# Performance work log

Measured on AMD Instinct MI355X. Metric: run time of the kernel, lower is better.

Reference implementation:

```python
import jax, jax.numpy as jnp
import numpy as np
from jax import lax

N, K, T_OBS, PRED = 64, 48, 30, 15
EMB, NODE, EDGE, ATT, CNN = 64, 128, 256, 64, 512


def setup_inputs():
    key = jax.random.key(0)
    ks = jax.random.split(key, 18)
    rn = lambda k, s, sc=1.0: jax.random.normal(k, s, jnp.float32) * sc
    return {
        "img_embedding": rn(ks[0], (N, CNN)),
        "target_obs_pos_abs": rn(ks[1], (N, T_OBS, 2)),
        "target_obs_pos_rel": rn(ks[2], (N, T_OBS, 2)),
        "target_obs_pos_step": rn(ks[3], (N, T_OBS, 2), 0.1),
        "nearby_obs_pos_abs": rn(ks[4], (N, K, T_OBS, 2)),
        "nearby_obs_pos_rel": rn(ks[5], (N, K, T_OBS, 2)),
        "nearby_obs_pos_step": rn(ks[6], (N, K, T_OBS, 2), 0.1),
        "target_obs_hist_size": jax.random.randint(ks[7], (N, 1), 0, T_OBS),
        "nearby_obs_hist_sizes": jax.random.randint(ks[8], (N, K, 1), 0, T_OBS),
        "W_disp": rn(ks[9], (EMB, 2), 0.1), "b_disp": jnp.zeros((EMB,), jnp.float32),
        "Wih_t": rn(ks[10], (4 * NODE, EMB), 0.05), "Whh_t": rn(ks[11], (4 * NODE, NODE), 0.05),
        "bih_t": jnp.zeros((4 * NODE,), jnp.float32), "bhh_t": jnp.zeros((4 * NODE,), jnp.float32),
        "Wih_n": rn(ks[12], (4 * EDGE, EMB), 0.05), "Whh_n": rn(ks[13], (4 * EDGE, EDGE), 0.05),
        "bih_n": jnp.zeros((4 * EDGE,), jnp.float32), "bhh_n": jnp.zeros((4 * EDGE,), jnp.float32),
        "W_att_t": rn(ks[14], (ATT, 2), 0.1), "b_att_t": jnp.zeros((ATT,), jnp.float32),
        "W_att_n": rn(ks[15], (ATT, 2), 0.1), "b_att_n": jnp.zeros((ATT,), jnp.float32),
        "W_pred": rn(ks[16], (2, NODE + CNN + EDGE), 0.02), "b_pred": jnp.zeros((2,), jnp.float32),
    }


def _lstm_cell(x, h, c, Wih, Whh, bih, bhh):
    # PyTorch LSTM gate order: i, f, g, o
    g = x @ Wih.T + h @ Whh.T + bih + bhh
    i, f, gg, o = jnp.split(g, 4, axis=-1)
    c2 = jax.nn.sigmoid(f) * c + jax.nn.sigmoid(i) * jnp.tanh(gg)
    return jax.nn.sigmoid(o) * jnp.tanh(c2), c2


def _forward(img_embedding, target_obs_pos_abs, target_obs_pos_rel, target_obs_pos_step,
             nearby_obs_pos_abs, nearby_obs_pos_rel, nearby_obs_pos_step,
             W_disp, b_disp, Wih_t, Whh_t, bih_t, bhh_t, Wih_n, Whh_n, bih_n, bhh_n,
             W_att_t, b_att_t, W_att_n, b_att_n, W_pred, b_pred,
             target_obs_hist_size, nearby_obs_hist_sizes):
    t_hist = target_obs_hist_size[:, 0]          # [N]
    n_hist = nearby_obs_hist_sizes[:, :, 0]      # [N, K]
    M = N * K

    def step(carry, t):
        tht, tct, nht, nct, Ht, cabs, crel, cstep, nabs, nstep = carry
        is_obs = t < T_OBS
        tc = jnp.minimum(t, T_OBS - 1)
        # prediction branch (only takes effect when t >= T_OBS)
        pred_out = jnp.concatenate([tht, img_embedding, Ht], 1) @ W_pred.T + b_pred  # [N,2]
        cabs = jnp.where(is_obs, target_obs_pos_abs[:, tc], cabs + pred_out)
        crel = jnp.where(is_obs, target_obs_pos_rel[:, tc], crel + pred_out)
        cstep = jnp.where(is_obs, target_obs_pos_step[:, tc], pred_out)
        nabs = jnp.where(is_obs, nearby_obs_pos_abs[:, :, tc], nabs)
        nstep = jnp.where(is_obs, nearby_obs_pos_step[:, :, tc], nstep)
        tmask = jnp.where(is_obs, t_hist > T_OBS - t, True)   # [N] bool
        nmask = jnp.where(is_obs, n_hist > T_OBS - t, True)   # [N,K] bool
        gate_t = jnp.sum(tmask) > 0  # emulates 'continue' when no target observed
        # target LSTM step, masked scatter-back
        th2, tc2 = _lstm_cell(cstep @ W_disp.T + b_disp, tht, tct, Wih_t, Whh_t, bih_t, bhh_t)
        u = (tmask & gate_t)[:, None]
        tht = jnp.where(u, th2, tht)
        tct = jnp.where(u, tc2, tct)
        # nearby LSTM step, masked scatter-back
        currN = jnp.sum(nmask)
        gate_n = gate_t & (currN > 0)
        nh2, nc2 = _lstm_cell(nstep.reshape(M, 2) @ W_disp.T + b_disp, nht, nct, Wih_n, Whh_n, bih_n, bhh_n)
        un = (nmask.reshape(M) & gate_n)[:, None]
        nht = jnp.where(un, nh2, nht)
        nct = jnp.where(un, nc2, nct)
        # social attention over padded nearby dim
        an = (nabs - cabs[:, None, :]) @ W_att_n.T + b_att_n   # [N,K,ATT]
        at = crel @ W_att_t.T + b_att_t                        # [N,ATT]
        mf = nmask.astype(jnp.float32)
        sc = jnp.einsum('nka,na->nk', an, at) * currN.astype(jnp.float32) / jnp.sqrt(jnp.float32(ATT))
        sc = sc * mf
        num = jnp.exp(sc - jnp.max(sc, 1, keepdims=True)) * mf
        w = num / (jnp.sum(num, 1, keepdims=True) + 1e-6)
        Ht = jnp.where(gate_n, jnp.einsum('nke,nk->ne', nht.reshape(N, K, EDGE), w), Ht)
        return (tht, tct, nht, nct, Ht, cabs, crel, cstep, nabs, nstep), crel

    z = lambda s: jnp.zeros(s, jnp.float32)
    init = (z((N, NODE)), z((N, NODE)), z((M, EDGE)), z((M, EDGE)), z((N, EDGE)),
            z((N, 2)), z((N, 2)), z((N, 2)), z((N, K, 2)), z((N, K, 2)))
    _, rels = lax.scan(step, init, jnp.arange(1, T_OBS + PRED))
    # last PRED emitted crel values are pred_traj[:, 0:PRED]
    return jnp.transpose(rels[-PRED:], (1, 0, 2))


def reference(img_embedding, target_obs_pos_abs, target_obs_pos_rel, target_obs_pos_step,
              nearby_obs_pos_abs, nearby_obs_pos_rel, nearby_obs_pos_step,
              target_obs_hist_size, nearby_obs_hist_sizes,
              W_disp, b_disp, Wih_t, Whh_t, bih_t, bhh_t, Wih_n, Whh_n, bih_n, bhh_n,
              W_att_t, b_att_t, W_att_n, b_att_n, W_pred, b_pred):
    return _forward(img_embedding, target_obs_pos_abs, target_obs_pos_rel, target_obs_pos_step,
                    nearby_obs_pos_abs, nearby_obs_pos_rel, nearby_obs_pos_step,
                    W_disp, b_disp, Wih_t, Whh_t, bih_t, bhh_t, Wih_n, Whh_n, bih_n, bhh_n,
                    W_att_t, b_att_t, W_att_n, b_att_n, W_pred, b_pred,
                    target_obs_hist_size, nearby_obs_hist_sizes)
```

## Files before the change

### kernel.cpp

```cpp
#include <hip/hip_runtime.h>
#include <math.h>

#define NT 64
#define KN 48
#define TOBS 30
#define NPRED 15
#define EMB 64
#define NODE 128
#define EDGE 256
#define ATTD 64
#define CNN 512
#define GNN 1024
#define GTT 512
#define KKA 320
#define TMAX 44

typedef _Float16 f16;
typedef f16 f16x8 __attribute__((ext_vector_type(8)));
typedef f16 f16x2 __attribute__((ext_vector_type(2)));
typedef float f32x4 __attribute__((ext_vector_type(4)));

__device__ __forceinline__ float rcp_f(float x) { return __builtin_amdgcn_rcpf(x); }
__device__ __forceinline__ float sigm(float x) { return rcp_f(1.f + __expf(-x)); }
__device__ __forceinline__ float tanh_f(float x) {
  float xx = fminf(fmaxf(x, -20.f), 20.f);
  float e = __expf(-2.f * xx);
  return (1.f - e) * rcp_f(1.f + e);
}
__device__ __forceinline__ unsigned ldcoh(const unsigned* p) {
  return __hip_atomic_load(p, __ATOMIC_RELAXED, __HIP_MEMORY_SCOPE_AGENT);
}
__device__ __forceinline__ float ldcohf(const float* p) {
  unsigned u = __hip_atomic_load((const unsigned*)p, __ATOMIC_RELAXED, __HIP_MEMORY_SCOPE_AGENT);
  return __builtin_bit_cast(float, u);
}
__device__ __forceinline__ void stcoh(unsigned* p, unsigned v) {
  __hip_atomic_store(p, v, __ATOMIC_RELAXED, __HIP_MEMORY_SCOPE_AGENT);
}
__device__ __forceinline__ void stcohf(float* p, float v) {
  __hip_atomic_store((unsigned*)p, __builtin_bit_cast(unsigned, v),
                     __ATOMIC_RELAXED, __HIP_MEMORY_SCOPE_AGENT);
}

__global__ __launch_bounds__(512) void prep_kernel(
    const float* __restrict__ Wih_n, const float* __restrict__ Whh_n,
    const float* __restrict__ bih_n, const float* __restrict__ bhh_n,
    const float* __restrict__ Wih_t, const float* __restrict__ Whh_t,
    const float* __restrict__ bih_t, const float* __restrict__ bhh_t,
    const int* __restrict__ t_hist, const int* __restrict__ n_hist,
    f16* __restrict__ Wn, f16* __restrict__ Wt,
    float* __restrict__ bias_n, float* __restrict__ bias_t,
    int* __restrict__ gt_arr, int* __restrict__ gn_arr, float* __restrict__ cn_arr,
    int* __restrict__ last29p, unsigned* __restrict__ flags)
{
  const int gid = blockIdx.x * 512 + threadIdx.x;
  const int nthr = gridDim.x * 512;
  __shared__ int sgn[TMAX + 1];

  if (gid < 2 * NT) flags[gid] = 0u;

  for (int idx = gid; idx < GNN * KKA; idx += nthr) {
    const int j    = idx & 7;
    const int lane = (idx >> 3) & 63;
    const int g    = (idx >> 9) & 3;
    const int r    = idx >> 11;
    const int kk   = r % 10;
    const int s    = r / 10;
    const int w    = s & 7;
    const int h    = s >> 3;
    const int col = g * 256 + h * 128 + w * 16 + (lane & 15);
    const int k   = kk * 32 + (lane >> 4) * 8 + j;
    const float v = (k < EMB) ? Wih_n[col * EMB + k] : Whh_n[col * EDGE + (k - EMB)];
    Wn[idx] = (f16)v;
  }
  for (int idx = gid; idx < GTT * 192; idx += nthr) {
    const int j = idx & 7;
    const int col = (idx >> 3) & 511;
    const int c8 = idx >> 12;
    const int k = c8 * 8 + j;
    const float v = (k < EMB) ? Wih_t[col * EMB + k] : Whh_t[col * NODE + (k - EMB)];
    Wt[idx] = (f16)v;
  }
  for (int idx = gid; idx < GNN; idx += nthr) bias_n[idx] = bih_n[idx] + bhh_n[idx];
  for (int idx = gid; idx < GTT; idx += nthr) bias_t[idx] = bih_t[idx] + bhh_t[idx];

  if (blockIdx.x == 0 && threadIdx.x < 352) {
    const int t = (threadIdx.x >> 3) + 1;
    const int part = threadIdx.x & 7;
    int any_t = 0, cnt = 0;
    if (t < TOBS) {
      const int thr = TOBS - t;
      for (int nn = part; nn < NT; nn += 8) any_t |= (t_hist[nn] > thr) ? 1 : 0;
      for (int m = part; m < NT * KN; m += 8) cnt += (n_hist[m] > thr) ? 1 : 0;
    } else { any_t = (part == 0); cnt = (part == 0) ? NT * KN : 0; }
    #pragma unroll
    for (int off = 1; off < 8; off <<= 1) {
      any_t |= __shfl_xor(any_t, off);
      cnt   += __shfl_xor(cnt, off);
    }
    if (part == 0) {
      const int gn = (any_t && cnt > 0) ? 1 : 0;
      gt_arr[t] = any_t;
      gn_arr[t] = gn;
      cn_arr[t] = (float)cnt;
      sgn[t] = gn;
    }
  }
  __syncthreads();
  if (blockIdx.x == 0 && threadIdx.x == 0) {
    int l = 30;
    for (int t = 29; t >= 1; --t) if (sgn[t]) { l = t; break; }
    last29p[0] = l;
  }
}

__global__ __launch_bounds__(512, 2) void model_kernel(
    const float* __restrict__ img, const float* __restrict__ tabs,
    const float* __restrict__ trel, const float* __restrict__ tstep,
    const float* __restrict__ nabs_g, const float* __restrict__ nstep_g,
    const int* __restrict__ thist_g, const int* __restrict__ nhist_g,
    const float* __restrict__ W_disp, const float* __restrict__ b_disp,
    const float* __restrict__ W_att_t, const float* __restrict__ b_att_t,
    const float* __restrict__ W_att_n, const float* __restrict__ b_att_n,
    const float* __restrict__ W_pred, const float* __restrict__ b_pred,
    const f16* __restrict__ Wn, const f16* __restrict__ Wt,
    const float* __restrict__ bias_n, const float* __restrict__ bias_t,
    const int* __restrict__ gt_arr, const int* __restrict__ gn_arr,
    const float* __restrict__ cn_arr, const int* __restrict__ last29p,
    unsigned* __restrict__ flags, unsigned* __restrict__ Hglob,
    float* __restrict__ Tglob,
    float* __restrict__ out)
{
  __shared__ f16 s_wlds[3 * 16384];
  __shared__ f16 Ax[KN][72];
  __shared__ f16 Ah[KN][264];
  __shared__ float s_tht[NODE];
  __shared__ float s_tct[64];
  __shared__ f16  s_th16[NODE];
  __shared__ float s_Ht[EDGE];
  __shared__ f16  s_x16[EMB];
  __shared__ float s_g[256];
  __shared__ float s_bt[256];
  __shared__ float s_at[ATTD];
  __shared__ float s_sc[KN], s_w[KN];
  __shared__ float s_scal[8];
  __shared__ float s_pimg[2];
  __shared__ int   s_nh[KN];
  __shared__ float s_wp[2][384];
  __shared__ float s_wan0[ATTD], s_wan1[ATTD], s_ban[ATTD];
  __shared__ float s_wat0[ATTD], s_wat1[ATTD], s_bat[ATTD];
  __shared__ float s_wd0[EMB], s_wd1[EMB], s_bd[EMB];

  const int tid  = threadIdx.x;
  const int n    = blockIdx.x & 63;
  const int hb   = blockIdx.x >> 6;
  const int w    = tid >> 6;
  const int lane = tid & 63;
  const int cl   = lane & 15;
  const int kq   = lane >> 4;
  const int koff = kq * 8;

  for (int i = tid; i < KN * 264; i += 512) ((f16*)Ah)[i] = (f16)0.f;
  for (int i = tid; i < NODE; i += 512) { s_tht[i] = 0.f; s_th16[i] = (f16)0.f; }
  if (tid < 64) s_tct[tid] = 0.f;
  for (int i = tid; i < EDGE; i += 512) s_Ht[i] = 0.f;
  if (tid < 256) {
    const int g = tid >> 6, dl = tid & 63;
    s_bt[tid] = bias_t[g * 128 + hb * 64 + dl];
  }
  for (int i = tid; i < 768; i += 512) {
    const int ww = i / 384, j = i - ww * 384;
    s_wp[ww][j] = (j < 128) ? W_pred[ww * 896 + j] : W_pred[ww * 896 + 640 + (j - 128)];
  }
  if (tid < KN) s_nh[tid] = nhist_g[n * KN + tid];
  if (tid < 8) s_scal[tid] = 0.f;
  if (tid >= 64 && tid < 128) {
    const int a = tid - 64;
    s_wan0[a] = W_att_n[a * 2]; s_wan1[a] = W_att_n[a * 2 + 1]; s_ban[a] = b_att_n[a];
  }
  if (tid >= 128 && tid < 192) {
    const int a = tid - 128;
    s_wat0[a] = W_att_t[a * 2]; s_wat1[a] = W_att_t[a * 2 + 1]; s_bat[a] = b_att_t[a];
  }
  if (tid >= 192 && tid < 256) {
    const int e = tid - 192;
    s_wd0[e] = W_disp[e * 2]; s_wd1[e] = W_disp[e * 2 + 1]; s_bd[e] = b_disp[e];
  }
  const int thist = thist_g[n];
  const int last29 = last29p[0];

  for (int i = tid; i < 3 * 8 * 256; i += 512) {
    const int c  = i & 255;
    const int wv = (i >> 8) & 7;
    const int kk = i >> 11;
    const size_t gbase = ((size_t)((hb * 8 + wv) * 10 + kk)) * 2048;
    *(f16x8*)(s_wlds + (size_t)(kk * 8 + wv) * 2048 + c * 8) =
        *(const f16x8*)(Wn + gbase + c * 8);
  }

  if (w < 2) {
    float s = 0.f;
    for (int j = lane; j < CNN; j += 64) s += img[n * CNN + j] * W_pred[w * 896 + 128 + j];
    for (int off = 32; off; off >>= 1) s += __shfl_down(s, off);
    if (lane == 0) s_pimg[w] = s + b_pred[w];
  }

  float creg[3][4];
  #pragma unroll
  for (int b = 0; b < 3; ++b)
    #pragma unroll
    for (int c = 0; c < 4; ++c) creg[b][c] = 0.f;

  float bias_q[4];
  #pragma unroll
  for (int g = 0; g < 4; ++g) bias_q[g] = bias_n[g * 256 + hb * 128 + w * 16 + cl];

  const f16* gW = Wn + ((size_t)(hb * 8 + w) * 10) * 2048 + (size_t)lane * 8;
  const f16* lW = s_wlds + (size_t)w * 2048 + (size_t)lane * 8;
  const int e_g = hb * 128 + w * 16 + cl;
  unsigned* myflag = flags + n * 2 + hb;
  unsigned* otflag = flags + n * 2 + (1 - hb);
  int bn = 0;

  __syncthreads();

  {
    for (int i = tid; i < KN * EMB; i += 512) {
      const int k = i >> 6, e = i & 63;
      const float s0 = nstep_g[((n * KN + k) * TOBS + 1) * 2 + 0];
      const float s1 = nstep_g[((n * KN + k) * TOBS + 1) * 2 + 1];
      Ax[k][e] = (f16)(s0 * s_wd0[e] + s1 * s_wd1[e] + s_bd[e]);
    }
    if (tid < 2) {
      s_scal[tid]     = tabs[(n * TOBS + 1) * 2 + tid];
      s_scal[2 + tid] = trel[(n * TOBS + 1) * 2 + tid];
      s_scal[4 + tid] = tstep[(n * TOBS + 1) * 2 + tid];
    }
    if (tid >= 448) {
      const int e = tid - 448;
      const float a0 = tstep[(n * TOBS + 1) * 2 + 0], a1 = tstep[(n * TOBS + 1) * 2 + 1];
      s_x16[e] = (f16)(a0 * s_wd0[e] + a1 * s_wd1[e] + s_bd[e]);
    }
    if (tid >= 384 && tid < 448) {
      const int a = tid - 384;
      const float r0 = trel[(n * TOBS + 1) * 2 + 0], r1 = trel[(n * TOBS + 1) * 2 + 1];
      s_at[a] = r0 * s_wat0[a] + r1 * s_wat1[a] + s_bat[a];
    }
  }
  __syncthreads();

  for (int t = 1; t <= TMAX; ++t) {
    const bool is_obs = (t < TOBS);
    const int tc = is_obs ? t : (TOBS - 1);
    const int gate_t = gt_arr[t];
    const int gate_n = gn_arr[t];
    const float currN = cn_arr[t];
    const bool tmask = is_obs ? (thist > (TOBS - t)) : true;
    const bool do_t = gate_t && tmask;
    const bool need_x = (gate_n || do_t);
    const bool do_att = gate_n && (t >= last29);
    const int par = bn & 1;

    if (!is_obs) {
      if (w < 2) {
        float s = 0.f;
        for (int j = lane; j < NODE; j += 64) s += s_tht[j] * s_wp[w][j];
        for (int j = lane; j < EDGE; j += 64) s += s_Ht[j] * s_wp[w][128 + j];
        for (int off = 32; off; off >>= 1) s += __shfl_down(s, off);
        if (lane == 0) {
          const float p = s + s_pimg[w];
          const float cabs = s_scal[w] + p;
          const float crel = s_scal[2 + w] + p;
          s_scal[w] = cabs; s_scal[2 + w] = crel; s_scal[4 + w] = p;
          if (hb == 0) out[(n * NPRED + (t - TOBS)) * 2 + w] = crel;
        }
      }
      __syncthreads();
      if (tid >= 448) {
        const int e = tid - 448;
        s_x16[e] = (f16)(s_scal[4] * s_wd0[e] + s_scal[5] * s_wd1[e] + s_bd[e]);
      }
      if (tid >= 384 && tid < 448) {
        const int a = tid - 384;
        s_at[a] = s_scal[2] * s_wat0[a] + s_scal[3] * s_wat1[a] + s_bat[a];
      }
      __syncthreads();
    }

    f16 hreg[3][4];
    if (gate_n) {
      f32x4 acc[3][4];
      #pragma unroll
      for (int rt = 0; rt < 3; ++rt)
        #pragma unroll
        for (int g = 0; g < 4; ++g) acc[rt][g] = (f32x4){0.f, 0.f, 0.f, 0.f};

      #pragma unroll
      for (int kk = 0; kk < 10; ++kk) {
        f16x8 bf[4];
        if (kk < 3) {
          #pragma unroll
          for (int g = 0; g < 4; ++g)
            bf[g] = *(const f16x8*)(lW + kk * 16384 + g * 512);
        } else {
          #pragma unroll
          for (int g = 0; g < 4; ++g)
            bf[g] = *(const f16x8*)(gW + kk * 2048 + g * 512);
        }
        f16x8 af[3];
        #pragma unroll
        for (int rt = 0; rt < 3; ++rt) {
          const int row = rt * 16 + cl;
          const f16* ap = (kk < 2) ? &Ax[row][kk * 32 + koff]
                                   : &Ah[row][(kk - 2) * 32 + koff];
          af[rt] = *(const f16x8*)ap;
        }
        #pragma unroll
        for (int g = 0; g < 4; ++g)
          #pragma unroll
          for (int rt = 0; rt < 3; ++rt)
            acc[rt][g] = __builtin_amdgcn_mfma_f32_16x16x32_f16(af[rt], bf[g], acc[rt][g], 0, 0, 0);
      }

      unsigned* Hg = Hglob + (size_t)(par * NT + n) * (KN * 128);
      #pragma unroll
      for (int rt = 0; rt < 3; ++rt) {
        #pragma unroll
        for (int jj = 0; jj < 4; ++jj) {
          const int row = rt * 16 + kq * 4 + jj;
          const bool nm = is_obs ? (s_nh[row] > (TOBS - t)) : true;
          f16 hv;
          if (nm) {
            const float iv = acc[rt][0][jj] + bias_q[0];
            const float fv = acc[rt][1][jj] + bias_q[1];
            const float gv = acc[rt][2][jj] + bias_q[2];
            const float ov = acc[rt][3][jj] + bias_q[3];
            const float c2 = sigm(fv) * creg[rt][jj] + sigm(iv) * tanh_f(gv);
            creg[rt][jj] = c2;
            hv = (f16)(sigm(ov) * tanh_f(c2));
          } else {
            hv = Ah[row][e_g];
          }
          hreg[rt][jj] = hv;
          const unsigned lo = (unsigned)__builtin_bit_cast(unsigned short, hv);
          const unsigned hi = (unsigned)__shfl_down((int)lo, 1);
          if (!(cl & 1))
            stcoh(Hg + row * 128 + (e_g >> 1), lo | (hi << 16));
        }
      }
    }

    if (do_t && tid < 256) {
      const int g = tid >> 6, dl = tid & 63;
      const int col = g * 128 + hb * 64 + dl;
      float g0 = s_bt[tid], g1 = 0.f, g2 = 0.f, g3 = 0.f;
      const f16x2* xt2 = (const f16x2*)s_x16;
      const f16x2* th2 = (const f16x2*)s_th16;
      const f16x8* wp = (const f16x8*)(Wt + col * 8);
      #pragma unroll
      for (int c8 = 0; c8 < 8; ++c8) {
        const f16x8 wv = wp[c8 * 512];
        f16x2 w0 = {wv[0], wv[1]}, w1 = {wv[2], wv[3]};
        f16x2 w2 = {wv[4], wv[5]}, w3 = {wv[6], wv[7]};
        g0 = __builtin_amdgcn_fdot2(w0, xt2[c8 * 4 + 0], g0, false);
        g1 = __builtin_amdgcn_fdot2(w1, xt2[c8 * 4 + 1], g1, false);
        g2 = __builtin_amdgcn_fdot2(w2, xt2[c8 * 4 + 2], g2, false);
        g3 = __builtin_amdgcn_fdot2(w3, xt2[c8 * 4 + 3], g3, false);
      }
      #pragma unroll
      for (int c8 = 8; c8 < 24; ++c8) {
        const f16x8 wv = wp[c8 * 512];
        f16x2 w0 = {wv[0], wv[1]}, w1 = {wv[2], wv[3]};
        f16x2 w2 = {wv[4], wv[5]}, w3 = {wv[6], wv[7]};
        g0 = __builtin_amdgcn_fdot2(w0, th2[(c8 - 8) * 4 + 0], g0, false);
        g1 = __builtin_amdgcn_fdot2(w1, th2[(c8 - 8) * 4 + 1], g1, false);
        g2 = __builtin_amdgcn_fdot2(w2, th2[(c8 - 8) * 4 + 2], g2, false);
        g3 = __builtin_amdgcn_fdot2(w3, th2[(c8 - 8) * 4 + 3], g3, false);
      }
      s_g[tid] = (g0 + g1) + (g2 + g3);
    }
    if (do_att && tid >= 256 && tid < 256 + KN) {
      const int k = tid - 256;
      const float a0 = nabs_g[((n * KN + k) * TOBS + tc) * 2 + 0] - s_scal[0];
      const float a1 = nabs_g[((n * KN + k) * TOBS + tc) * 2 + 1] - s_scal[1];
      const bool nm = is_obs ? (s_nh[k] > (TOBS - t)) : true;
      float c0 = 0.f, c1 = 0.f, c2 = 0.f, c3 = 0.f;
      #pragma unroll 4
      for (int a = 0; a < ATTD; a += 4) {
        c0 += (a0 * s_wan0[a]     + a1 * s_wan1[a]     + s_ban[a])     * s_at[a];
        c1 += (a0 * s_wan0[a + 1] + a1 * s_wan1[a + 1] + s_ban[a + 1]) * s_at[a + 1];
        c2 += (a0 * s_wan0[a + 2] + a1 * s_wan1[a + 2] + s_ban[a + 2]) * s_at[a + 2];
        c3 += (a0 * s_wan0[a + 3] + a1 * s_wan1[a + 3] + s_ban[a + 3]) * s_at[a + 3];
      }
      float sc = ((c0 + c1) + (c2 + c3)) * currN * 0.125f;
      s_sc[k] = nm ? sc : 0.f;
      s_w[k]  = nm ? 1.f : 0.f;
    }
    __syncthreads();

    if (do_t && tid < 64) {
      const int d = hb * 64 + tid;
      const float iv = s_g[tid], fv = s_g[64 + tid];
      const float gv = s_g[128 + tid], ov = s_g[192 + tid];
      const float c2 = sigm(fv) * s_tct[tid] + sigm(iv) * tanh_f(gv);
      s_tct[tid] = c2;
      const float nh = sigm(ov) * tanh_f(c2);
      s_tht[d] = nh;
      s_th16[d] = (f16)nh;
      stcohf(Tglob + ((size_t)(par * NT + n) * 2 + hb) * 64 + tid, nh);
    }
    if (do_att && w == 4) {
      const bool act = lane < KN;
      const float sc = act ? s_sc[lane] : -1.0e30f;
      const float mf = act ? s_w[lane] : 0.f;
      float mx = sc;
      #pragma unroll
      for (int off = 32; off; off >>= 1) mx = fmaxf(mx, __shfl_xor(mx, off));
      float num = __expf(sc - mx) * mf;
      float sum = num;
      #pragma unroll
      for (int off = 32; off; off >>= 1) sum += __shfl_xor(sum, off);
      if (act) s_w[lane] = num * rcp_f(sum + 1e-6f);
    }
    __syncthreads();

    if (need_x && tid == 0) {
      stcoh(myflag, (unsigned)(bn + 1));
    }

    {
      const int tn = t + 1;
      if (tn <= TOBS) {
        const int tcn = (tn < TOBS) ? tn : (TOBS - 1);
        for (int i = tid; i < KN * EMB; i += 512) {
          const int k = i >> 6, e = i & 63;
          const float s0 = nstep_g[((n * KN + k) * TOBS + tcn) * 2 + 0];
          const float s1 = nstep_g[((n * KN + k) * TOBS + tcn) * 2 + 1];
          Ax[k][e] = (f16)(s0 * s_wd0[e] + s1 * s_wd1[e] + s_bd[e]);
        }
      }
      if (tn < TOBS) {
        if (tid < 2) {
          s_scal[tid]     = tabs[(n * TOBS + tn) * 2 + tid];
          s_scal[2 + tid] = trel[(n * TOBS + tn) * 2 + tid];
          s_scal[4 + tid] = tstep[(n * TOBS + tn) * 2 + tid];
        }
        if (tid >= 448) {
          const int e = tid - 448;
          const float a0 = tstep[(n * TOBS + tn) * 2 + 0], a1 = tstep[(n * TOBS + tn) * 2 + 1];
          s_x16[e] = (f16)(a0 * s_wd0[e] + a1 * s_wd1[e] + s_bd[e]);
        }
        if (tid >= 384 && tid < 448) {
          const int a = tid - 384;
          const float r0 = trel[(n * TOBS + tn) * 2 + 0], r1 = trel[(n * TOBS + tn) * 2 + 1];
          s_at[a] = r0 * s_wat0[a] + r1 * s_wat1[a] + s_bat[a];
        }
      }
    }

    if (need_x && tid == 0) {
      const unsigned step = (unsigned)(bn + 1);
      while (ldcoh(otflag) < step)
        __builtin_amdgcn_s_sleep(1);
    }
    __syncthreads();

    if (gate_n) {
      const unsigned* Hg = Hglob + (size_t)(par * NT + n) * (KN * 128);
      const int ob = (1 - hb) * 64;
      for (int i = tid; i < KN * 64; i += 512) {
        const int row = i >> 6, c = i & 63;
        const unsigned v = ldcoh(Hg + row * 128 + ob + c);
        *(unsigned*)&Ah[row][(ob + c) * 2] = v;
      }
      #pragma unroll
      for (int rt = 0; rt < 3; ++rt)
        #pragma unroll
        for (int jj = 0; jj < 4; ++jj)
          Ah[rt * 16 + kq * 4 + jj][e_g] = hreg[rt][jj];
    }
    if (do_t && tid >= 448) {
      const int dl = tid - 448;
      const int d = (1 - hb) * 64 + dl;
      const float nh = ldcohf(Tglob + ((size_t)(par * NT + n) * 2 + (1 - hb)) * 64 + dl);
      s_tht[d] = nh;
      s_th16[d] = (f16)nh;
    }
    __syncthreads();

    if (do_att && tid < EDGE) {
      float h0 = 0.f, h1 = 0.f, h2 = 0.f, h3 = 0.f;
      #pragma unroll
      for (int k = 0; k < KN; k += 4) {
        h0 += (float)Ah[k][tid]     * s_w[k];
        h1 += (float)Ah[k + 1][tid] * s_w[k + 1];
        h2 += (float)Ah[k + 2][tid] * s_w[k + 2];
        h3 += (float)Ah[k + 3][tid] * s_w[k + 3];
      }
      s_Ht[tid] = (h0 + h1) + (h2 + h3);
    }
    if (need_x) bn++;
    if (t >= 29) __syncthreads();
  }
}

extern "C" void kernel_launch(void* const* d_in, const int* in_sizes, int n_in,
                              void* d_out, int out_size, void* d_ws, size_t ws_size,
                              hipStream_t stream) {
  const float* img    = (const float*)d_in[0];
  const float* tabs   = (const float*)d_in[1];
  const float* trel   = (const float*)d_in[2];
  const float* tstep  = (const float*)d_in[3];
  const float* nabs   = (const float*)d_in[4];
  const float* nstep  = (const float*)d_in[6];
  const int*   thist  = (const int*)d_in[7];
  const int*   nhist  = (const int*)d_in[8];
  const float* W_disp = (const float*)d_in[9];
  const float* b_disp = (const float*)d_in[10];
  const float* Wih_t  = (const float*)d_in[11];
  const float* Whh_t  = (const float*)d_in[12];
  const float* bih_t  = (const float*)d_in[13];
  const float* bhh_t  = (const float*)d_in[14];
  const float* Wih_n  = (const float*)d_in[15];
  const float* Whh_n  = (const float*)d_in[16];
  const float* bih_n  = (const float*)d_in[17];
  const float* bhh_n  = (const float*)d_in[18];
  const float* W_att_t = (const float*)d_in[19];
  const float* b_att_t = (const float*)d_in[20];
  const float* W_att_n = (const float*)d_in[21];
  const float* b_att_n = (const float*)d_in[22];
  const float* W_pred  = (const float*)d_in[23];
  const float* b_pred  = (const float*)d_in[24];

  char* ws = (char*)d_ws;
  f16*      Wn      = (f16*)(ws);
  f16*      Wt      = (f16*)(ws + 655360);
  float*    bias_n  = (float*)(ws + 851968);
  float*    bias_t  = (float*)(ws + 856064);
  int*      gt_arr  = (int*)(ws + 858112);
  int*      gn_arr  = (int*)(ws + 858304);
  float*    cn_arr  = (float*)(ws + 858496);
  int*      last29p = (int*)(ws + 859648);
  unsigned* flags   = (unsigned*)(ws + 860160);
  unsigned* Hglob   = (unsigned*)(ws + 1048576);
  float*    Tglob   = (float*)(ws + 4194304);

  prep_kernel<<<64, 512, 0, stream>>>(Wih_n, Whh_n, bih_n, bhh_n, Wih_t, Whh_t,
                                      bih_t, bhh_t, thist, nhist, Wn, Wt,
                                      bias_n, bias_t, gt_arr, gn_arr, cn_arr,
                                      last29p, flags);
  model_kernel<<<2 * NT, 512, 0, stream>>>(img, tabs, trel, tstep, nabs, nstep,
                                           thist, nhist, W_disp, b_disp,
                                           W_att_t, b_att_t, W_att_n, b_att_n,
                                           W_pred, b_pred,
                                           Wn, Wt, bias_n, bias_t,
                                           gt_arr, gn_arr, cn_arr, last29p,
                                           flags, Hglob, Tglob,
                                           (float*)d_out);
}
```

Before: 718.4 us.

## Fold displacement embedding into LSTM input weights and collapse attention dot

Precomputes W_ih·W_disp and W_ih·b_disp in the prep kernel, so the neighbor LSTM input GEMM takes a 3-wide raw step vector (padded to one 32-wide K tile) instead of a 64-wide embedding. This removes one K-tile from the per-step MFMA loop and the per-step embedding fill of the Ax buffer. The target LSTM also uses precomputed projected vectors. The attention score is rewritten by first reducing the target attention vector against the neighbor attention weights, so each neighbor costs a 3-term dot instead of a 64-length loop. Rounding changes slightly because composed weights are stored in fp16.

```diff
diff --git a/kernel.cpp b/kernel.cpp
--- a/kernel.cpp
+++ b/kernel.cpp
@@ -12,7 +12,6 @@
 #define CNN 512
 #define GNN 1024
 #define GTT 512
-#define KKA 320
 #define TMAX 44
 
 typedef _Float16 f16;
@@ -47,8 +46,9 @@
     const float* __restrict__ bih_n, const float* __restrict__ bhh_n,
     const float* __restrict__ Wih_t, const float* __restrict__ Whh_t,
     const float* __restrict__ bih_t, const float* __restrict__ bhh_t,
+    const float* __restrict__ W_disp, const float* __restrict__ b_disp,
     const int* __restrict__ t_hist, const int* __restrict__ n_hist,
-    f16* __restrict__ Wn, f16* __restrict__ Wt,
+    f16* __restrict__ Wn, f16* __restrict__ Wt, float* __restrict__ Ptv,
     float* __restrict__ bias_n, float* __restrict__ bias_t,
     int* __restrict__ gt_arr, int* __restrict__ gn_arr, float* __restrict__ cn_arr,
     int* __restrict__ last29p, unsigned* __restrict__ flags)
@@ -59,18 +59,31 @@
 
   if (gid < 2 * NT) flags[gid] = 0u;
 
-  for (int idx = gid; idx < GNN * KKA; idx += nthr) {
+  for (int idx = gid; idx < GNN * 288; idx += nthr) {
     const int j    = idx & 7;
     const int lane = (idx >> 3) & 63;
     const int g    = (idx >> 9) & 3;
     const int r    = idx >> 11;
-    const int kk   = r % 10;
-    const int s    = r / 10;
+    const int u    = r % 9;
+    const int s    = r / 9;
     const int w    = s & 7;
     const int h    = s >> 3;
     const int col = g * 256 + h * 128 + w * 16 + (lane & 15);
-    const int k   = kk * 32 + (lane >> 4) * 8 + j;
-    const float v = (k < EMB) ? Wih_n[col * EMB + k] : Whh_n[col * EDGE + (k - EMB)];
+    float v = 0.f;
+    if (u == 0) {
+      if ((lane >> 4) == 0 && j < 3) {
+        float acc = 0.f;
+        for (int e = 0; e < EMB; ++e) {
+          const float sel = (j == 0) ? W_disp[e * 2]
+                          : (j == 1) ? W_disp[e * 2 + 1] : b_disp[e];
+          acc += sel * Wih_n[col * EMB + e];
+        }
+        v = acc;
+      }
+    } else {
+      const int k = (u - 1) * 32 + (lane >> 4) * 8 + j;
+      v = Whh_n[col * EDGE + k];
+    }
     Wn[idx] = (f16)v;
   }
   for (int idx = gid; idx < GTT * 192; idx += nthr) {
@@ -80,6 +93,17 @@
     const int k = c8 * 8 + j;
     const float v = (k < EMB) ? Wih_t[col * EMB + k] : Whh_t[col * NODE + (k - EMB)];
     Wt[idx] = (f16)v;
+  }
+  for (int idx = gid; idx < 3 * GTT; idx += nthr) {
+    const int sel = idx / GTT;
+    const int col = idx - sel * GTT;
+    float acc = 0.f;
+    for (int e = 0; e < EMB; ++e) {
+      const float sv = (sel == 0) ? W_disp[e * 2]
+                     : (sel == 1) ? W_disp[e * 2 + 1] : b_disp[e];
+      acc += sv * Wih_t[col * EMB + e];
+    }
+    Ptv[sel * GTT + col] = acc;
   }
   for (int idx = gid; idx < GNN; idx += nthr) bias_n[idx] = bih_n[idx] + bhh_n[idx];
   for (int idx = gid; idx < GTT; idx += nthr) bias_t[idx] = bih_t[idx] + bhh_t[idx];
@@ -119,11 +143,11 @@
     const float* __restrict__ trel, const float* __restrict__ tstep,
     const float* __restrict__ nabs_g, const float* __restrict__ nstep_g,
     const int* __restrict__ thist_g, const int* __restrict__ nhist_g,
-    const float* __restrict__ W_disp, const float* __restrict__ b_disp,
     const float* __restrict__ W_att_t, const float* __restrict__ b_att_t,
     const float* __restrict__ W_att_n, const float* __restrict__ b_att_n,
     const float* __restrict__ W_pred, const float* __restrict__ b_pred,
     const f16* __restrict__ Wn, const f16* __restrict__ Wt,
+    const float* __restrict__ Ptv,
     const float* __restrict__ bias_n, const float* __restrict__ bias_t,
     const int* __restrict__ gt_arr, const int* __restrict__ gn_arr,
     const float* __restrict__ cn_arr, const int* __restrict__ last29p,
@@ -132,24 +156,22 @@
     float* __restrict__ out)
 {
   __shared__ f16 s_wlds[3 * 16384];
-  __shared__ f16 Ax[KN][72];
+  __shared__ f16 s_virt[KN][32];
   __shared__ f16 Ah[KN][264];
   __shared__ float s_tht[NODE];
   __shared__ float s_tct[64];
   __shared__ f16  s_th16[NODE];
   __shared__ float s_Ht[EDGE];
-  __shared__ f16  s_x16[EMB];
   __shared__ float s_g[256];
   __shared__ float s_bt[256];
-  __shared__ float s_at[ATTD];
   __shared__ float s_sc[KN], s_w[KN];
   __shared__ float s_scal[8];
+  __shared__ float s_dd[4];
   __shared__ float s_pimg[2];
   __shared__ int   s_nh[KN];
   __shared__ float s_wp[2][384];
   __shared__ float s_wan0[ATTD], s_wan1[ATTD], s_ban[ATTD];
   __shared__ float s_wat0[ATTD], s_wat1[ATTD], s_bat[ATTD];
-  __shared__ float s_wd0[EMB], s_wd1[EMB], s_bd[EMB];
 
   const int tid  = threadIdx.x;
   const int n    = blockIdx.x & 63;
@@ -161,6 +183,8 @@
   const int koff = kq * 8;
 
   for (int i = tid; i < KN * 264; i += 512) ((f16*)Ah)[i] = (f16)0.f;
+  for (int i = tid; i < KN * 32; i += 512)
+    s_virt[i >> 5][i & 31] = ((i & 31) == 2) ? (f16)1.f : (f16)0.f;
   for (int i = tid; i < NODE; i += 512) { s_tht[i] = 0.f; s_th16[i] = (f16)0.f; }
   if (tid < 64) s_tct[tid] = 0.f;
   for (int i = tid; i < EDGE; i += 512) s_Ht[i] = 0.f;
@@ -182,19 +206,21 @@
     const int a = tid - 128;
     s_wat0[a] = W_att_t[a * 2]; s_wat1[a] = W_att_t[a * 2 + 1]; s_bat[a] = b_att_t[a];
   }
-  if (tid >= 192 && tid < 256) {
-    const int e = tid - 192;
-    s_wd0[e] = W_disp[e * 2]; s_wd1[e] = W_disp[e * 2 + 1]; s_bd[e] = b_disp[e];
-  }
   const int thist = thist_g[n];
   const int last29 = last29p[0];
+
+  float pt0 = 0.f, pt1 = 0.f, ptb = 0.f;
+  if (tid < 256) {
+    const int col = (tid >> 6) * 128 + hb * 64 + (tid & 63);
+    pt0 = Ptv[col]; pt1 = Ptv[512 + col]; ptb = Ptv[1024 + col];
+  }
 
   for (int i = tid; i < 3 * 8 * 256; i += 512) {
     const int c  = i & 255;
     const int wv = (i >> 8) & 7;
-    const int kk = i >> 11;
-    const size_t gbase = ((size_t)((hb * 8 + wv) * 10 + kk)) * 2048;
-    *(f16x8*)(s_wlds + (size_t)(kk * 8 + wv) * 2048 + c * 8) =
+    const int u  = i >> 11;
+    const size_t gbase = ((size_t)((hb * 8 + wv) * 9 + u)) * 2048;
+    *(f16x8*)(s_wlds + (size_t)(u * 8 + wv) * 2048 + c * 8) =
         *(const f16x8*)(Wn + gbase + c * 8);
   }
 
@@ -215,7 +241,7 @@
   #pragma unroll
   for (int g = 0; g < 4; ++g) bias_q[g] = bias_n[g * 256 + hb * 128 + w * 16 + cl];
 
-  const f16* gW = Wn + ((size_t)(hb * 8 + w) * 10) * 2048 + (size_t)lane * 8;
+  const f16* gW = Wn + ((size_t)(hb * 8 + w) * 9) * 2048 + (size_t)lane * 8;
   const f16* lW = s_wlds + (size_t)w * 2048 + (size_t)lane * 8;
   const int e_g = hb * 128 + w * 16 + cl;
   unsigned* myflag = flags + n * 2 + hb;
@@ -225,26 +251,25 @@
   __syncthreads();
 
   {
-    for (int i = tid; i < KN * EMB; i += 512) {
-      const int k = i >> 6, e = i & 63;
-      const float s0 = nstep_g[((n * KN + k) * TOBS + 1) * 2 + 0];
-      const float s1 = nstep_g[((n * KN + k) * TOBS + 1) * 2 + 1];
-      Ax[k][e] = (f16)(s0 * s_wd0[e] + s1 * s_wd1[e] + s_bd[e]);
+    if (tid < 96) {
+      const int row = tid >> 1, comp = tid & 1;
+      s_virt[row][comp] = (f16)nstep_g[((n * KN + row) * TOBS + 1) * 2 + comp];
     }
     if (tid < 2) {
       s_scal[tid]     = tabs[(n * TOBS + 1) * 2 + tid];
       s_scal[2 + tid] = trel[(n * TOBS + 1) * 2 + tid];
       s_scal[4 + tid] = tstep[(n * TOBS + 1) * 2 + tid];
     }
-    if (tid >= 448) {
-      const int e = tid - 448;
-      const float a0 = tstep[(n * TOBS + 1) * 2 + 0], a1 = tstep[(n * TOBS + 1) * 2 + 1];
-      s_x16[e] = (f16)(a0 * s_wd0[e] + a1 * s_wd1[e] + s_bd[e]);
-    }
     if (tid >= 384 && tid < 448) {
       const int a = tid - 384;
       const float r0 = trel[(n * TOBS + 1) * 2 + 0], r1 = trel[(n * TOBS + 1) * 2 + 1];
-      s_at[a] = r0 * s_wat0[a] + r1 * s_wat1[a] + s_bat[a];
+      const float at = r0 * s_wat0[a] + r1 * s_wat1[a] + s_bat[a];
+      float p0 = at * s_wan0[a], p1 = at * s_wan1[a], pb = at * s_ban[a];
+      #pragma unroll
+      for (int off = 32; off; off >>= 1) {
+        p0 += __shfl_xor(p0, off); p1 += __shfl_xor(p1, off); pb += __shfl_xor(pb, off);
+      }
+      if (a == 0) { s_dd[0] = p0; s_dd[1] = p1; s_dd[2] = pb; }
     }
   }
   __syncthreads();
@@ -276,13 +301,15 @@
         }
       }
       __syncthreads();
-      if (tid >= 448) {
-        const int e = tid - 448;
-        s_x16[e] = (f16)(s_scal[4] * s_wd0[e] + s_scal[5] * s_wd1[e] + s_bd[e]);
-      }
       if (tid >= 384 && tid < 448) {
         const int a = tid - 384;
-        s_at[a] = s_scal[2] * s_wat0[a] + s_scal[3] * s_wat1[a] + s_bat[a];
+        const float at = s_scal[2] * s_wat0[a] + s_scal[3] * s_wat1[a] + s_bat[a];
+        float p0 = at * s_wan0[a], p1 = at * s_wan1[a], pb = at * s_ban[a];
+        #pragma unroll
+        for (int off = 32; off; off >>= 1) {
+          p0 += __shfl_xor(p0, off); p1 += __shfl_xor(p1, off); pb += __shfl_xor(pb, off);
+        }
+        if (a == 0) { s_dd[0] = p0; s_dd[1] = p1; s_dd[2] = pb; }
       }
       __syncthreads();
     }
@@ -296,23 +323,23 @@
         for (int g = 0; g < 4; ++g) acc[rt][g] = (f32x4){0.f, 0.f, 0.f, 0.f};
 
       #pragma unroll
-      for (int kk = 0; kk < 10; ++kk) {
+      for (int u = 0; u < 9; ++u) {
         f16x8 bf[4];
-        if (kk < 3) {
+        if (u < 3) {
           #pragma unroll
           for (int g = 0; g < 4; ++g)
-            bf[g] = *(const f16x8*)(lW + kk * 16384 + g * 512);
+            bf[g] = *(const f16x8*)(lW + u * 16384 + g * 512);
         } else {
           #pragma unroll
           for (int g = 0; g < 4; ++g)
-            bf[g] = *(const f16x8*)(gW + kk * 2048 + g * 512);
+            bf[g] = *(const f16x8*)(gW + u * 2048 + g * 512);
         }
         f16x8 af[3];
         #pragma unroll
         for (int rt = 0; rt < 3; ++rt) {
           const int row = rt * 16 + cl;
-          const f16* ap = (kk < 2) ? &Ax[row][kk * 32 + koff]
-                                   : &Ah[row][(kk - 2) * 32 + koff];
+          const f16* ap = (u == 0) ? &s_virt[row][koff]
+                                   : &Ah[row][(u - 1) * 32 + koff];
           af[rt] = *(const f16x8*)ap;
         }
         #pragma unroll
@@ -351,31 +378,19 @@
     }
 
     if (do_t && tid < 256) {
-      const int g = tid >> 6, dl = tid & 63;
-      const int col = g * 128 + hb * 64 + dl;
-      float g0 = s_bt[tid], g1 = 0.f, g2 = 0.f, g3 = 0.f;
-      const f16x2* xt2 = (const f16x2*)s_x16;
+      float g0 = s_bt[tid] + s_scal[4] * pt0 + s_scal[5] * pt1 + ptb;
+      float g1 = 0.f, g2 = 0.f, g3 = 0.f;
       const f16x2* th2 = (const f16x2*)s_th16;
-      const f16x8* wp = (const f16x8*)(Wt + col * 8);
-      #pragma unroll
-      for (int c8 = 0; c8 < 8; ++c8) {
-        const f16x8 wv = wp[c8 * 512];
+      const f16x8* wp = (const f16x8*)(Wt + ((tid >> 6) * 128 + hb * 64 + (tid & 63)) * 8);
+      #pragma unroll
+      for (int c8 = 0; c8 < 16; ++c8) {
+        const f16x8 wv = wp[(c8 + 8) * 512];
         f16x2 w0 = {wv[0], wv[1]}, w1 = {wv[2], wv[3]};
         f16x2 w2 = {wv[4], wv[5]}, w3 = {wv[6], wv[7]};
-        g0 = __builtin_amdgcn_fdot2(w0, xt2[c8 * 4 + 0], g0, false);
-        g1 = __builtin_amdgcn_fdot2(w1, xt2[c8 * 4 + 1], g1, false);
-        g2 = __builtin_amdgcn_fdot2(w2, xt2[c8 * 4 + 2], g2, false);
-        g3 = __builtin_amdgcn_fdot2(w3, xt2[c8 * 4 + 3], g3, false);
-      }
-      #pragma unroll
-      for (int c8 = 8; c8 < 24; ++c8) {
-        const f16x8 wv = wp[c8 * 512];
-        f16x2 w0 = {wv[0], wv[1]}, w1 = {wv[2], wv[3]};
-        f16x2 w2 = {wv[4], wv[5]}, w3 = {wv[6], wv[7]};
-        g0 = __builtin_amdgcn_fdot2(w0, th2[(c8 - 8) * 4 + 0], g0, false);
-        g1 = __builtin_amdgcn_fdot2(w1, th2[(c8 - 8) * 4 + 1], g1, false);
-        g2 = __builtin_amdgcn_fdot2(w2, th2[(c8 - 8) * 4 + 2], g2, false);
-        g3 = __builtin_amdgcn_fdot2(w3, th2[(c8 - 8) * 4 + 3], g3, false);
+        g0 = __builtin_amdgcn_fdot2(w0, th2[c8 * 4 + 0], g0, false);
+        g1 = __builtin_amdgcn_fdot2(w1, th2[c8 * 4 + 1], g1, false);
+        g2 = __builtin_amdgcn_fdot2(w2, th2[c8 * 4 + 2], g2, false);
+        g3 = __builtin_amdgcn_fdot2(w3, th2[c8 * 4 + 3], g3, false);
       }
       s_g[tid] = (g0 + g1) + (g2 + g3);
     }
@@ -384,15 +399,7 @@
       const float a0 = nabs_g[((n * KN + k) * TOBS + tc) * 2 + 0] - s_scal[0];
       const float a1 = nabs_g[((n * KN + k) * TOBS + tc) * 2 + 1] - s_scal[1];
       const bool nm = is_obs ? (s_nh[k] > (TOBS - t)) : true;
-      float c0 = 0.f, c1 = 0.f, c2 = 0.f, c3 = 0.f;
-      #pragma unroll 4
-      for (int a = 0; a < ATTD; a += 4) {
-        c0 += (a0 * s_wan0[a]     + a1 * s_wan1[a]     + s_ban[a])     * s_at[a];
-        c1 += (a0 * s_wan0[a + 1] + a1 * s_wan1[a + 1] + s_ban[a + 1]) * s_at[a + 1];
-        c2 += (a0 * s_wan0[a + 2] + a1 * s_wan1[a + 2] + s_ban[a + 2]) * s_at[a + 2];
-        c3 += (a0 * s_wan0[a + 3] + a1 * s_wan1[a + 3] + s_ban[a + 3]) * s_at[a + 3];
-      }
-      float sc = ((c0 + c1) + (c2 + c3)) * currN * 0.125f;
+      const float sc = (a0 * s_dd[0] + a1 * s_dd[1] + s_dd[2]) * currN * 0.125f;
       s_sc[k] = nm ? sc : 0.f;
       s_w[k]  = nm ? 1.f : 0.f;
     }
@@ -432,11 +439,9 @@
       const int tn = t + 1;
       if (tn <= TOBS) {
         const int tcn = (tn < TOBS) ? tn : (TOBS - 1);
-        for (int i = tid; i < KN * EMB; i += 512) {
-          const int k = i >> 6, e = i & 63;
-          const float s0 = nstep_g[((n * KN + k) * TOBS + tcn) * 2 + 0];
-          const float s1 = nstep_g[((n * KN + k) * TOBS + tcn) * 2 + 1];
-          Ax[k][e] = (f16)(s0 * s_wd0[e] + s1 * s_wd1[e] + s_bd[e]);
+        if (tid < 96) {
+          const int row = tid >> 1, comp = tid & 1;
+          s_virt[row][comp] = (f16)nstep_g[((n * KN + row) * TOBS + tcn) * 2 + comp];
         }
       }
       if (tn < TOBS) {
@@ -445,15 +450,16 @@
           s_scal[2 + tid] = trel[(n * TOBS + tn) * 2 + tid];
           s_scal[4 + tid] = tstep[(n * TOBS + tn) * 2 + tid];
         }
-        if (tid >= 448) {
-          const int e = tid - 448;
-          const float a0 = tstep[(n * TOBS + tn) * 2 + 0], a1 = tstep[(n * TOBS + tn) * 2 + 1];
-          s_x16[e] = (f16)(a0 * s_wd0[e] + a1 * s_wd1[e] + s_bd[e]);
-        }
         if (tid >= 384 && tid < 448) {
           const int a = tid - 384;
           const float r0 = trel[(n * TOBS + tn) * 2 + 0], r1 = trel[(n * TOBS + tn) * 2 + 1];
-          s_at[a] = r0 * s_wat0[a] + r1 * s_wat1[a] + s_bat[a];
+          const float at = r0 * s_wat0[a] + r1 * s_wat1[a] + s_bat[a];
+          float p0 = at * s_wan0[a], p1 = at * s_wan1[a], pb = at * s_ban[a];
+          #pragma unroll
+          for (int off = 32; off; off >>= 1) {
+            p0 += __shfl_xor(p0, off); p1 += __shfl_xor(p1, off); pb += __shfl_xor(pb, off);
+          }
+          if (a == 0) { s_dd[0] = p0; s_dd[1] = p1; s_dd[2] = pb; }
         }
       }
     }
@@ -542,18 +548,20 @@
   float*    cn_arr  = (float*)(ws + 858496);
   int*      last29p = (int*)(ws + 859648);
   unsigned* flags   = (unsigned*)(ws + 860160);
+  float*    Ptv     = (float*)(ws + 901120);
   unsigned* Hglob   = (unsigned*)(ws + 1048576);
   float*    Tglob   = (float*)(ws + 4194304);
 
   prep_kernel<<<64, 512, 0, stream>>>(Wih_n, Whh_n, bih_n, bhh_n, Wih_t, Whh_t,
-                                      bih_t, bhh_t, thist, nhist, Wn, Wt,
+                                      bih_t, bhh_t, W_disp, b_disp,
+                                      thist, nhist, Wn, Wt, Ptv,
                                       bias_n, bias_t, gt_arr, gn_arr, cn_arr,
                                       last29p, flags);
   model_kernel<<<2 * NT, 512, 0, stream>>>(img, tabs, trel, tstep, nabs, nstep,
-                                           thist, nhist, W_disp, b_disp,
+                                           thist, nhist,
                                            W_att_t, b_att_t, W_att_n, b_att_n,
                                            W_pred, b_pred,
-                                           Wn, Wt, bias_n, bias_t,
+                                           Wn, Wt, Ptv, bias_n, bias_t,
                                            gt_arr, gn_arr, cn_arr, last29p,
                                            flags, Hglob, Tglob,
                                            (float*)d_out);
```

New measurement: 634.6 us. -11.7%, faster.
